# Kernel optimization log

Measured on AMD Instinct MI355X. Metric: run time of the kernel, lower is better.

Reference implementation:

```python
import jax, jax.numpy as jnp
import numpy as np
from jax import lax

EPS = 1e-5
F_CH = 32  # TIM future channels = int(256/8)
B_CH = 32  # TIM past channels (note: source bug -> these are zeroed, not shifted)


def inorm(x):
    # InstanceNorm3d (no affine): normalize each (b, c) over (T, H, W), biased var
    m = jnp.mean(x, axis=(2, 3, 4), keepdims=True)
    v = jnp.var(x, axis=(2, 3, 4), keepdims=True)
    return (x - m) * lax.rsqrt(v + EPS)


def conv1x1(x, w):
    # pointwise conv: x [B,C,T,H,W], w [O,C]
    return jnp.einsum('bcthw,oc->bothw', x, w)


def dwconv(x, w, pad):
    # depthwise 3D conv; w [C,1,kd,kh,kw], pad = [(pd,pd),(ph,ph),(pw,pw)]
    return lax.conv_general_dilated(
        x, w, window_strides=(1, 1, 1), padding=pad,
        feature_group_count=x.shape[1],
        dimension_numbers=('NCDHW', 'OIDHW', 'NCDHW'))


def tim(x):
    # Non-circular temporal interlacing. Faithful to source (past slice is a no-op):
    # channels [0:f]  <- x shifted from future (t+1), zero-padded at last frame
    # channels [f:f+b] <- zeros
    # channels [f+b:] <- identity
    f, b = F_CH, B_CH
    fut = jnp.concatenate([x[:, :f, 1:], jnp.zeros_like(x[:, :f, :1])], axis=2)
    mid = jnp.zeros_like(x[:, f:f + b])
    return jnp.concatenate([fut, mid, x[:, f + b:]], axis=1)


def setup_inputs() -> dict:
    key = jax.random.key(0)
    ks = jax.random.split(key, 7)
    cin, hid, cout = 64, 256, 64
    x = jax.random.normal(ks[0], (4, cin, 16, 64, 64), dtype=jnp.float32)
    w1 = jax.random.normal(ks[1], (hid, cin), dtype=jnp.float32) * 0.05
    w_dw_s = jax.random.normal(ks[2], (hid, 1, 1, 3, 3), dtype=jnp.float32) * 0.1
    w_dw_t = jax.random.normal(ks[3], (hid, 1, 3, 1, 1), dtype=jnp.float32) * 0.1
    w_se1 = jax.random.normal(ks[4], (hid // 4, hid), dtype=jnp.float32) * 0.05
    w_se2 = jax.random.normal(ks[5], (hid, hid // 4), dtype=jnp.float32) * 0.05
    w_proj = jax.random.normal(ks[6], (cout, hid), dtype=jnp.float32) * 0.05
    return {'x': x, 'w1': w1, 'w_dw_s': w_dw_s, 'w_dw_t': w_dw_t,
            'w_se1': w_se1, 'w_se2': w_se2, 'w_proj': w_proj}


def reference(x, w1, w_dw_s, w_dw_t, w_se1, w_se2, w_proj):
    shortcut = x
    # stage1: expand 1x1 conv + IN + ReLU
    h = jax.nn.relu(inorm(conv1x1(x, w1)))
    # temporal interlace (zero-FLOP channel shift)
    h = tim(h)
    # stage2: depthwise spatial (1,3,3) + IN + ReLU
    h = jax.nn.relu(inorm(dwconv(h, w_dw_s, [(0, 0), (1, 1), (1, 1)])))
    # stage3: depthwise temporal (3,1,1) + IN + ReLU
    h = jax.nn.relu(inorm(dwconv(h, w_dw_t, [(1, 1), (0, 0), (0, 0)])))
    # squeeze-excite
    y = jnp.mean(h, axis=(2, 3, 4), keepdims=True)           # [B,C,1,1,1]
    y = jax.nn.relu(jnp.einsum('bcthw,oc->bothw', y, w_se1))
    y = jax.nn.sigmoid(jnp.einsum('bcthw,oc->bothw', y, w_se2))
    h = h * y
    # proj 1x1 + IN, residual, maxpool (1,2,2)
    out = inorm(conv1x1(h, w_proj)) + shortcut
    out = lax.reduce_window(out, -jnp.inf, lax.max,
                            (1, 1, 1, 2, 2), (1, 1, 1, 2, 2), 'VALID')
    return out
```

## Files before the change

kernel.cpp:

```cpp
#include <hip/hip_runtime.h>
#include <hip/hip_bf16.h>

#define B_   4
#define CIN  64
#define HID  256
#define COUT 64
#define T_   16
#define H_   64
#define W_   64
#define HW_  (H_*W_)
#define THW  (T_*HW_)
#define EPS  1e-5f

typedef unsigned short ushort_t;
typedef unsigned int   uint_t;
typedef short bf16x8 __attribute__((ext_vector_type(8)));
typedef float f32x4  __attribute__((ext_vector_type(4)));

#define SM3   4096
#define SIS3  5120
#define SSES  6144
#define SAL   7168
#define SBE   8192
__device__ float g_stats[10240];
__device__ float g_eps [4*1024*256];
__device__ float g_epss[4*1024*256];
__device__ float g_pps [4*64*512];
__device__ float g_ppss[4*64*512];
__device__ ushort_t g_wpack[32768];

__device__ __forceinline__ float bf2f(ushort_t u) {
    return __uint_as_float(((uint_t)u) << 16);
}
__device__ __forceinline__ ushort_t f2bf(float f) {
    uint_t u = __float_as_uint(f);
    uint_t r = u + 0x7fffu + ((u >> 16) & 1u);
    return (ushort_t)(r >> 16);
}
__device__ __forceinline__ void unpacknorm2(uint2 k, float a, float bb, float* v) {
    uint_t uu[2] = {k.x, k.y};
    #pragma unroll
    for (int j = 0; j < 2; ++j) {
        v[2*j]   = fmaxf(fmaf(__uint_as_float(uu[j] << 16),         a, bb), 0.f);
        v[2*j+1] = fmaxf(fmaf(__uint_as_float(uu[j] & 0xffff0000u), a, bb), 0.f);
    }
}

__global__ __launch_bounds__(256) void k_prep(const float* __restrict__ w1,
                                              const float* __restrict__ wproj) {
    int idx = blockIdx.x*256 + threadIdx.x;
    {
        int j = idx & 7, lane = (idx>>3) & 63, ot = (idx>>9) & 3;
        int ks = (idx>>11) & 1, wv = idx >> 12;
        int ln = lane & 15, q = lane >> 4;
        int o = wv*64 + ot*16 + ln, k = ks*32 + q*8 + j;
        g_wpack[idx] = f2bf(w1[o*CIN + k]);
    }
    {
        int j = idx & 7, lane = (idx>>3) & 63, ot = (idx>>9) & 3, kg = idx >> 11;
        int ln = lane & 15, q = lane >> 4;
        int o = ot*16 + ln, k = kg*32 + q*8 + j;
        g_wpack[16384 + idx] = f2bf(wproj[o*HID + k]);
    }
}

__global__ __launch_bounds__(256) void k_expand(const float* __restrict__ x,
                                                ushort_t* __restrict__ h1, int b0) {
    union SMem {
        ushort_t Bs[64*72];
        float    red[2][256][16];
    };
    __shared__ SMem sm;
    const int tid = threadIdx.x;
    const int bb  = blockIdx.y, gb = b0 + bb;
    const int pos0 = blockIdx.x * 64;
    const int lane = tid & 63, wv = tid >> 6;
    const int q = lane >> 4, ln = lane & 15;

    bf16x8 af[2][4];
    #pragma unroll
    for (int ks = 0; ks < 2; ++ks)
        #pragma unroll
        for (int ot = 0; ot < 4; ++ot)
            af[ks][ot] = *(const bf16x8*)&g_wpack[(((wv*2+ks)*4+ot)<<9) + lane*8];

    #pragma unroll
    for (int i = 0; i < 4; ++i) {
        int lin = i*1024 + tid*4;
        int k = lin >> 6, n0 = lin & 63;
        float4 v = *(const float4*)&x[(size_t)(gb*CIN + k) * THW + pos0 + n0];
        ushort_t* d = &sm.Bs[k*72 + ((n0 + 16*((k>>3)&3)) & 63)];
        d[0] = f2bf(v.x); d[1] = f2bf(v.y); d[2] = f2bf(v.z); d[3] = f2bf(v.w);
    }
    __syncthreads();

    f32x4 acc[4][4];
    #pragma unroll
    for (int i = 0; i < 4; ++i)
        #pragma unroll
        for (int j = 0; j < 4; ++j)
            acc[i][j] = (f32x4){0.f,0.f,0.f,0.f};

    #pragma unroll
    for (int ks = 0; ks < 2; ++ks) {
        bf16x8 bfr[4];
        #pragma unroll
        for (int nt = 0; nt < 4; ++nt) {
            union { short s[8]; bf16x8 v; } bu;
            #pragma unroll
            for (int j = 0; j < 8; ++j) {
                int k = ks*32 + q*8 + j;
                int nn = (nt*16 + ln + 16*((k>>3)&3)) & 63;
                bu.s[j] = (short)sm.Bs[k*72 + nn];
            }
            bfr[nt] = bu.v;
        }
        #pragma unroll
        for (int ot = 0; ot < 4; ++ot)
            #pragma unroll
            for (int nt = 0; nt < 4; ++nt)
                acc[ot][nt] = __builtin_amdgcn_mfma_f32_16x16x32_bf16(
                    af[ks][ot], bfr[nt], acc[ot][nt], 0, 0, 0);
    }

    float sp_[16], ssp_[16];
    #pragma unroll
    for (int i = 0; i < 16; ++i) { sp_[i] = 0.f; ssp_[i] = 0.f; }

    #pragma unroll
    for (int ot = 0; ot < 4; ++ot)
        #pragma unroll
        for (int nt = 0; nt < 4; ++nt)
            #pragma unroll
            for (int r = 0; r < 4; ++r) {
                float vv = acc[ot][nt][r];
                int o = wv*64 + ot*16 + q*4 + r;
                int n = nt*16 + ln;
                h1[((size_t)bb*HID + o)*THW + pos0 + n] = f2bf(vv);
                sp_[ot*4+r] += vv;
                ssp_[ot*4+r] = fmaf(vv, vv, ssp_[ot*4+r]);
            }

    __syncthreads();
    #pragma unroll
    for (int i = 0; i < 16; ++i) {
        int o = wv*64 + (i>>2)*16 + q*4 + (i&3);
        sm.red[0][o][ln] = sp_[i];
        sm.red[1][o][ln] = ssp_[i];
    }
    __syncthreads();
    {
        float s = 0.f, ss = 0.f;
        #pragma unroll
        for (int l = 0; l < 16; ++l) {
            s  += sm.red[0][tid][l];
            ss += sm.red[1][tid][l];
        }
        size_t base = ((size_t)bb*1024 + blockIdx.x)*256 + tid;
        g_eps [base] = s;
        g_epss[base] = ss;
    }
}

__global__ __launch_bounds__(1024) void k_mid(const ushort_t* __restrict__ h1,
                                              const float* __restrict__ wdws,
                                              const float* __restrict__ wdwt,
                                              ushort_t* __restrict__ h3) {
    const int tid = threadIdx.x;
    const int bc  = blockIdx.x;
    const int o   = bc & (HID-1);
    const int bb  = bc >> 8;
    const int wid = tid >> 6, lane = tid & 63;

    if (o >= 32 && o < 64) {
        if (tid == 0) {
            g_stats[SM3  + bc] = 0.f;
            g_stats[SIS3 + bc] = 1.f / sqrtf(EPS);
            g_stats[SSES + bc] = 0.f;
        }
        return;
    }

    __shared__ float pl[2][66*67];
    __shared__ float ls[16], lss[16];
    __shared__ float sa, sb;

    {
        const float* ps  = &g_eps [((size_t)bb*1024)*256 + o];
        const float* pss = &g_epss[((size_t)bb*1024)*256 + o];
        float s  = ps [(size_t)tid*256];
        float ss = pss[(size_t)tid*256];
        #pragma unroll
        for (int m = 32; m > 0; m >>= 1) {
            s  += __shfl_xor(s,  m);
            ss += __shfl_xor(ss, m);
        }
        if (lane == 0) { ls[wid] = s; lss[wid] = ss; }
        if (tid < 66) {
            #pragma unroll
            for (int b = 0; b < 2; ++b) {
                pl[b][tid]         = 0.f;
                pl[b][65*67 + tid] = 0.f;
                pl[b][tid*67]      = 0.f;
                pl[b][tid*67 + 65] = 0.f;
            }
        }
        __syncthreads();
        if (tid == 0) {
            float st = 0.f, sst = 0.f;
            #pragma unroll
            for (int i = 0; i < 16; ++i) { st += ls[i]; sst += lss[i]; }
            float m = st * (1.f/THW);
            float v = sst * (1.f/THW) - m*m;
            float is = 1.f / sqrtf(v + EPS);
            sa = is; sb = -m * is;
        }
        __syncthreads();
    }
    const float a1 = sa, b1 = sb;

    const int fut = (o < 32) ? 1 : 0;
    const int y   = tid >> 4;
    const int x0  = (tid & 15) * 4;
    const ushort_t* chp = h1 + (size_t)bc * THW;
    const int lastp = fut ? (T_-2) : (T_-1);

    float wf[9];
    #pragma unroll
    for (int k = 0; k < 9; ++k) wf[k] = wdws[o*9 + k];

    uint2 sreg[2];
    sreg[0] = *(const uint2*)(chp + (size_t)fut*HW_ + tid*4);
    {
        float vv[4];
        unpacknorm2(sreg[0], a1, b1, vv);
        float* dst = &pl[0][(y+1)*67 + x0 + 1];
        #pragma unroll
        for (int i = 0; i < 4; ++i) dst[i] = vv[i];
    }
    sreg[1] = *(const uint2*)(chp + (size_t)(1+fut)*HW_ + tid*4);
    __syncthreads();

    uint2 keep[16];
    float s2 = 0.f, ss2 = 0.f;

    #pragma unroll
    for (int t = 0; t < T_; ++t) {
        if (t + 2 <= lastp)
            sreg[t & 1] = *(const uint2*)(chp + (size_t)(t+2+fut)*HW_ + tid*4);
        if (t + 1 <= lastp) {
            float vv[4];
            unpacknorm2(sreg[(t+1) & 1], a1, b1, vv);
            float* dst = &pl[(t+1) & 1][(y+1)*67 + x0 + 1];
            #pragma unroll
            for (int i = 0; i < 4; ++i) dst[i] = vv[i];
        }
        if (fut && t == T_-1) {
            keep[t] = (uint2){0u, 0u};
        } else {
            const float* plane = pl[t & 1];
            float v[3][6];
            #pragma unroll
            for (int dy = 0; dy < 3; ++dy) {
                const float* rp = &plane[(y + dy)*67 + x0];
                #pragma unroll
                for (int j = 0; j < 6; ++j) v[dy][j] = rp[j];
            }
            uint_t outp[2];
            #pragma unroll
            for (int i2 = 0; i2 < 2; ++i2) {
                float o0 = 0.f, o1 = 0.f;
                #pragma unroll
                for (int dy = 0; dy < 3; ++dy)
                    #pragma unroll
                    for (int dx = 0; dx < 3; ++dx) {
                        float w = wf[dy*3+dx];
                        o0 = fmaf(w, v[dy][2*i2 + dx],     o0);
                        o1 = fmaf(w, v[dy][2*i2 + 1 + dx], o1);
                    }
                ushort_t u0 = f2bf(o0), u1 = f2bf(o1);
                float r0 = bf2f(u0), r1 = bf2f(u1);
                s2 += r0 + r1; ss2 = fmaf(r0, r0, fmaf(r1, r1, ss2));
                outp[i2] = (uint_t)u0 | ((uint_t)u1 << 16);
            }
            keep[t].x = outp[0]; keep[t].y = outp[1];
        }
        __syncthreads();
    }

    {
        float s = s2, ss = ss2;
        #pragma unroll
        for (int m = 32; m > 0; m >>= 1) {
            s  += __shfl_xor(s,  m);
            ss += __shfl_xor(ss, m);
        }
        if (lane == 0) { ls[wid] = s; lss[wid] = ss; }
        __syncthreads();
        if (tid == 0) {
            float st = 0.f, sst = 0.f;
            #pragma unroll
            for (int i = 0; i < 16; ++i) { st += ls[i]; sst += lss[i]; }
            float m = st * (1.f/THW);
            float v = sst * (1.f/THW) - m*m;
            float is = 1.f / sqrtf(v + EPS);
            sa = is; sb = -m * is;
        }
        __syncthreads();
    }
    const float a2 = sa, b2 = sb;

    const float w0 = wdwt[o*3+0], w1 = wdwt[o*3+1], w2 = wdwt[o*3+2];
    ushort_t* op = h3 + (size_t)bc * THW + tid*4;

    float p[4], c[4], n[4];
    #pragma unroll
    for (int i = 0; i < 4; ++i) p[i] = 0.f;
    unpacknorm2(keep[0], a2, b2, c);
    unpacknorm2(keep[1], a2, b2, n);

    float s3 = 0.f, ss3 = 0.f;
    #pragma unroll
    for (int t = 0; t < T_; ++t) {
        uint_t outp[2];
        #pragma unroll
        for (int i2 = 0; i2 < 2; ++i2) {
            float o0 = fmaf(w0, p[2*i2],   fmaf(w1, c[2*i2],   w2 * n[2*i2]));
            float o1 = fmaf(w0, p[2*i2+1], fmaf(w1, c[2*i2+1], w2 * n[2*i2+1]));
            ushort_t u0 = f2bf(o0), u1 = f2bf(o1);
            float r0 = bf2f(u0), r1 = bf2f(u1);
            s3 += r0 + r1; ss3 = fmaf(r0, r0, fmaf(r1, r1, ss3));
            outp[i2] = (uint_t)u0 | ((uint_t)u1 << 16);
        }
        uint2 r; r.x = outp[0]; r.y = outp[1];
        *(uint2*)(op + (size_t)t*HW_) = r;

        #pragma unroll
        for (int i = 0; i < 4; ++i) { p[i] = c[i]; c[i] = n[i]; }
        if (t + 2 < T_) unpacknorm2(keep[t+2], a2, b2, n);
        else {
            #pragma unroll
            for (int i = 0; i < 4; ++i) n[i] = 0.f;
        }
        keep[t] = r;
    }

    {
        float s = s3, ss = ss3;
        #pragma unroll
        for (int m = 32; m > 0; m >>= 1) {
            s  += __shfl_xor(s,  m);
            ss += __shfl_xor(ss, m);
        }
        if (lane == 0) { ls[wid] = s; lss[wid] = ss; }
        __syncthreads();
        if (tid == 0) {
            float st = 0.f, sst = 0.f;
            #pragma unroll
            for (int i = 0; i < 16; ++i) { st += ls[i]; sst += lss[i]; }
            float m = st * (1.f/THW);
            float v = sst * (1.f/THW) - m*m;
            float is = 1.f / sqrtf(v + EPS);
            g_stats[SM3  + bc] = m;
            g_stats[SIS3 + bc] = is;
            sa = is; sb = -m * is;
        }
        __syncthreads();
    }

    const float a3 = sa, b3 = sb;
    float sse = 0.f;
    #pragma unroll
    for (int t = 0; t < T_; ++t) {
        uint_t uu[2] = {keep[t].x, keep[t].y};
        #pragma unroll
        for (int j = 0; j < 2; ++j) {
            sse += fmaxf(fmaf(__uint_as_float(uu[j] << 16),         a3, b3), 0.f);
            sse += fmaxf(fmaf(__uint_as_float(uu[j] & 0xffff0000u), a3, b3), 0.f);
        }
    }
    #pragma unroll
    for (int m = 32; m > 0; m >>= 1) sse += __shfl_xor(sse, m);
    if (lane == 0) ls[wid] = sse;
    __syncthreads();
    if (tid == 0) {
        float st = 0.f;
        #pragma unroll
        for (int i = 0; i < 16; ++i) st += ls[i];
        g_stats[SSES + bc] = st * (1.f/THW);
    }
}

__global__ __launch_bounds__(256) void k_semlp(const float* __restrict__ wse1,
                                               const float* __restrict__ wse2) {
    __shared__ float mv[HID];
    __shared__ float y1[64];
    const int bb = blockIdx.x, tid = threadIdx.x;
    mv[tid] = g_stats[SSES + bb*HID + tid];
    __syncthreads();
    if (tid < 64) {
        float acc = 0.f;
        #pragma unroll 8
        for (int c = 0; c < HID; ++c) acc = fmaf(wse1[tid*HID + c], mv[c], acc);
        y1[tid] = fmaxf(acc, 0.f);
    }
    __syncthreads();
    float z = 0.f;
    #pragma unroll
    for (int c = 0; c < 64; ++c) z = fmaf(wse2[tid*64 + c], y1[c], z);
    float se = 1.f / (1.f + expf(-z));
    const int bc = bb*HID + tid;
    float al = g_stats[SIS3 + bc] * se;
    if (tid >= 32 && tid < 64) al = 0.f;
    g_stats[SAL + bc] = al;
    g_stats[SBE + bc] = -g_stats[SM3 + bc] * al;
}

__global__ __launch_bounds__(256) void k_proj(const ushort_t* __restrict__ h3,
                                              float* __restrict__ proj) {
    __shared__ ushort_t Bs[64*136];
    __shared__ float rs[64][4], rss[64][4];
    const int tid = threadIdx.x;
    const int bb  = blockIdx.y;
    const int pos0 = blockIdx.x * 128;
    const int lane = tid & 63, wv = tid >> 6;
    const int q = lane >> 4, ln = lane & 15;

    f32x4 acc[4][2];
    #pragma unroll
    for (int i = 0; i < 4; ++i) {
        acc[i][0] = (f32x4){0.f,0.f,0.f,0.f};
        acc[i][1] = (f32x4){0.f,0.f,0.f,0.f};
    }

    for (int kc = 0; kc < 4; ++kc) {
        #pragma unroll
        for (int i = 0; i < 8; ++i) {
            int lin = i*1024 + tid*4;
            int kl = lin >> 7, n0 = lin & 127;
            int ch = bb*HID + kc*64 + kl;
            float al = g_stats[SAL + ch], be = g_stats[SBE + ch];
            ushort_t* d = &Bs[kl*136 + ((n0 + 16*((kl>>3)&7)) & 127)];
            if (al == 0.f) {
                d[0] = 0; d[1] = 0; d[2] = 0; d[3] = 0;
            } else {
                uint2 u = *(const uint2*)&h3[(size_t)ch * THW + pos0 + n0];
                float f0 = __uint_as_float(u.x << 16);
                float f1 = __uint_as_float(u.x & 0xffff0000u);
                float f2 = __uint_as_float(u.y << 16);
                float f3 = __uint_as_float(u.y & 0xffff0000u);
                d[0] = f2bf(fmaxf(fmaf(f0, al, be), 0.f));
                d[1] = f2bf(fmaxf(fmaf(f1, al, be), 0.f));
                d[2] = f2bf(fmaxf(fmaf(f2, al, be), 0.f));
                d[3] = f2bf(fmaxf(fmaf(f3, al, be), 0.f));
            }
        }
        __syncthreads();

        #pragma unroll
        for (int ks = 0; ks < 2; ++ks) {
            int kg = kc*2 + ks;
            bf16x8 af[4];
            #pragma unroll
            for (int ot = 0; ot < 4; ++ot)
                af[ot] = *(const bf16x8*)&g_wpack[16384 + ((kg*4+ot)<<9) + lane*8];
            bf16x8 bfr[2];
            #pragma unroll
            for (int nt = 0; nt < 2; ++nt) {
                union { short s[8]; bf16x8 v; } bu;
                #pragma unroll
                for (int j = 0; j < 8; ++j) {
                    int kl = ks*32 + q*8 + j;
                    int nn = (wv*32 + nt*16 + ln + 16*((kl>>3)&7)) & 127;
                    bu.s[j] = (short)Bs[kl*136 + nn];
                }
                bfr[nt] = bu.v;
            }
            #pragma unroll
            for (int ot = 0; ot < 4; ++ot)
                #pragma unroll
                for (int nt = 0; nt < 2; ++nt)
                    acc[ot][nt] = __builtin_amdgcn_mfma_f32_16x16x32_bf16(
                        af[ot], bfr[nt], acc[ot][nt], 0, 0, 0);
        }
        __syncthreads();
    }

    #pragma unroll
    for (int ot = 0; ot < 4; ++ot)
        #pragma unroll
        for (int nt = 0; nt < 2; ++nt)
            #pragma unroll
            for (int r = 0; r < 4; ++r) {
                int o = ot*16 + q*4 + r;
                int n = wv*32 + nt*16 + ln;
                proj[((size_t)bb*COUT + o)*THW + pos0 + n] = acc[ot][nt][r];
            }

    #pragma unroll
    for (int ot = 0; ot < 4; ++ot)
        #pragma unroll
        for (int r = 0; r < 4; ++r) {
            float s  = acc[ot][0][r] + acc[ot][1][r];
            float ss = fmaf(acc[ot][0][r], acc[ot][0][r],
                            acc[ot][1][r] * acc[ot][1][r]);
            #pragma unroll
            for (int m = 1; m < 16; m <<= 1) {
                s  += __shfl_xor(s,  m);
                ss += __shfl_xor(ss, m);
            }
            if (ln == 0) {
                int o = ot*16 + q*4 + r;
                rs[o][wv]  = s;
                rss[o][wv] = ss;
            }
        }
    __syncthreads();
    if (tid < 64) {
        float s  = rs[tid][0]  + rs[tid][1]  + rs[tid][2]  + rs[tid][3];
        float ss = rss[tid][0] + rss[tid][1] + rss[tid][2] + rss[tid][3];
        size_t base = ((size_t)bb*64 + tid)*512 + blockIdx.x;
        g_pps [base] = s;
        g_ppss[base] = ss;
    }
}

__global__ __launch_bounds__(1024) void k_final(const float* __restrict__ proj,
                                                const float* __restrict__ x,
                                                float* __restrict__ out, int b0) {
    const int bo  = blockIdx.x;
    const int tid = threadIdx.x;
    const float* p = proj + (size_t)bo * THW;

    float s = 0.f, ss = 0.f;
    if (tid < 512) {
        s  = g_pps [(size_t)bo*512 + tid];
        ss = g_ppss[(size_t)bo*512 + tid];
    }
    #pragma unroll
    for (int off = 32; off > 0; off >>= 1) {
        s  += __shfl_down(s,  off, 64);
        ss += __shfl_down(ss, off, 64);
    }
    __shared__ float ls[16], lss[16];
    __shared__ float sa, sb;
    int wid = tid >> 6, lane = tid & 63;
    if (lane == 0) { ls[wid] = s; lss[wid] = ss; }
    __syncthreads();
    if (tid == 0) {
        float st = 0.f, sst = 0.f;
        #pragma unroll
        for (int i = 0; i < 16; ++i) { st += ls[i]; sst += lss[i]; }
        float m = st * (1.f/THW);
        float v = sst * (1.f/THW) - m*m;
        float is = 1.f / sqrtf(v + EPS);
        sa = is; sb = -m * is;
    }
    __syncthreads();
    const float a = sa, bb = sb;

    const size_t gbase = (size_t)(b0*COUT + bo) * THW;
    float* op = out + (size_t)(b0*COUT + bo) * (T_*1024);
    #pragma unroll
    for (int i = 0; i < 16; ++i) {
        int idx = i*1024 + tid;
        int xx = idx & 31, yy = (idx >> 5) & 31, t = idx >> 10;
        float m = -3.4e38f;
        #pragma unroll
        for (int r = 0; r < 2; ++r) {
            size_t off = (size_t)t*HW_ + (size_t)(2*yy + r)*W_ + 2*xx;
            float2 p2 = *(const float2*)(p + off);
            float2 x2 = *(const float2*)(x + gbase + off);
            float v0 = fmaf(p2.x, a, bb) + x2.x;
            float v1 = fmaf(p2.y, a, bb) + x2.y;
            m = fmaxf(m, fmaxf(v0, v1));
        }
        op[idx] = m;
    }
}

extern "C" void kernel_launch(void* const* d_in, const int* in_sizes, int n_in,
                              void* d_out, int out_size, void* d_ws, size_t ws_size,
                              hipStream_t stream) {
    const float* x     = (const float*)d_in[0];
    const float* w1    = (const float*)d_in[1];
    const float* wdws  = (const float*)d_in[2];
    const float* wdwt  = (const float*)d_in[3];
    const float* wse1  = (const float*)d_in[4];
    const float* wse2  = (const float*)d_in[5];
    const float* wproj = (const float*)d_in[6];
    float* out = (float*)d_out;

    const size_t perb = 2ull * HID * THW * sizeof(ushort_t);
    int nb = (ws_size >= 4*perb) ? 4 : (ws_size >= 2*perb) ? 2 : 1;

    k_prep<<<64, 256, 0, stream>>>(w1, wproj);

    for (int b0 = 0; b0 < B_; b0 += nb) {
        char* ws = (char*)d_ws;
        ushort_t* h1   = (ushort_t*)ws;
        ushort_t* h3   = h1;
        float*    proj = (float*)(ws + (size_t)nb * HID*THW*2);

        k_expand<<<dim3(THW/64, nb), 256, 0, stream>>>(x, h1, b0);
        k_mid   <<<nb*HID, 1024, 0, stream>>>(h1, wdws, wdwt, h3);
        k_semlp <<<nb, 256, 0, stream>>>(wse1, wse2);
        k_proj  <<<dim3(THW/128, nb), 256, 0, stream>>>(h3, proj);
        k_final <<<nb*COUT, 1024, 0, stream>>>(proj, x, out, b0);
    }
}
```

Before: 376.3 us.

## Move stage-1 stat reduction to separate kernel and recompute proj stats in final

Adds a k_red kernel that reduces the per-block expand partial sums into per-channel normalization scale and shift before k_mid, so the 1024-thread k_mid blocks no longer each do a strided gather and two block barriers. k_proj no longer computes and writes partial sums of its output. k_final instead recomputes the mean and variance by re-reading the whole projection channel from memory. This trades an extra launch and an extra pass over the proj data for a lighter GEMM epilogue and a lighter k_mid prologue.

```diff
diff --git a/kernel.cpp b/kernel.cpp
--- a/kernel.cpp
+++ b/kernel.cpp
@@ -17,6 +17,8 @@
 typedef short bf16x8 __attribute__((ext_vector_type(8)));
 typedef float f32x4  __attribute__((ext_vector_type(4)));
 
+#define SA1   0
+#define SB1   1024
 #define SM3   4096
 #define SIS3  5120
 #define SSES  6144
@@ -25,8 +27,6 @@
 __device__ float g_stats[10240];
 __device__ float g_eps [4*1024*256];
 __device__ float g_epss[4*1024*256];
-__device__ float g_pps [4*64*512];
-__device__ float g_ppss[4*64*512];
 __device__ ushort_t g_wpack[32768];
 
 __device__ __forceinline__ float bf2f(ushort_t u) {
@@ -162,6 +162,37 @@
     }
 }
 
+__global__ __launch_bounds__(256) void k_red() {
+    const int tid = threadIdx.x;
+    const int cg  = blockIdx.x;
+    const int bb  = blockIdx.y;
+    const int ch  = cg*16 + (tid & 15);
+    const int pb0 = tid >> 4;
+    const float* ps  = &g_eps [((size_t)bb*1024)*256];
+    const float* pss = &g_epss[((size_t)bb*1024)*256];
+    float s = 0.f, ss = 0.f;
+    #pragma unroll 8
+    for (int it = 0; it < 64; ++it) {
+        int pb = it*16 + pb0;
+        s  += ps [(size_t)pb*256 + ch];
+        ss += pss[(size_t)pb*256 + ch];
+    }
+    __shared__ float rs[256], rss[256];
+    rs[tid] = s; rss[tid] = ss;
+    __syncthreads();
+    if (tid < 16) {
+        float st = 0.f, sst = 0.f;
+        #pragma unroll
+        for (int k = 0; k < 16; ++k) { st += rs[tid + 16*k]; sst += rss[tid + 16*k]; }
+        float m = st * (1.f/THW);
+        float v = sst * (1.f/THW) - m*m;
+        float is = 1.f / sqrtf(v + EPS);
+        int bc = bb*HID + cg*16 + tid;
+        g_stats[SA1 + bc] = is;
+        g_stats[SB1 + bc] = -m * is;
+    }
+}
+
 __global__ __launch_bounds__(1024) void k_mid(const ushort_t* __restrict__ h1,
                                               const float* __restrict__ wdws,
                                               const float* __restrict__ wdwt,
@@ -185,39 +216,18 @@
     __shared__ float ls[16], lss[16];
     __shared__ float sa, sb;
 
-    {
-        const float* ps  = &g_eps [((size_t)bb*1024)*256 + o];
-        const float* pss = &g_epss[((size_t)bb*1024)*256 + o];
-        float s  = ps [(size_t)tid*256];
-        float ss = pss[(size_t)tid*256];
-        #pragma unroll
-        for (int m = 32; m > 0; m >>= 1) {
-            s  += __shfl_xor(s,  m);
-            ss += __shfl_xor(ss, m);
-        }
-        if (lane == 0) { ls[wid] = s; lss[wid] = ss; }
-        if (tid < 66) {
-            #pragma unroll
-            for (int b = 0; b < 2; ++b) {
-                pl[b][tid]         = 0.f;
-                pl[b][65*67 + tid] = 0.f;
-                pl[b][tid*67]      = 0.f;
-                pl[b][tid*67 + 65] = 0.f;
-            }
-        }
-        __syncthreads();
-        if (tid == 0) {
-            float st = 0.f, sst = 0.f;
-            #pragma unroll
-            for (int i = 0; i < 16; ++i) { st += ls[i]; sst += lss[i]; }
-            float m = st * (1.f/THW);
-            float v = sst * (1.f/THW) - m*m;
-            float is = 1.f / sqrtf(v + EPS);
-            sa = is; sb = -m * is;
-        }
-        __syncthreads();
-    }
-    const float a1 = sa, b1 = sb;
+    const float a1 = g_stats[SA1 + bc];
+    const float b1 = g_stats[SB1 + bc];
+
+    if (tid < 66) {
+        #pragma unroll
+        for (int b = 0; b < 2; ++b) {
+            pl[b][tid]         = 0.f;
+            pl[b][65*67 + tid] = 0.f;
+            pl[b][tid*67]      = 0.f;
+            pl[b][tid*67 + 65] = 0.f;
+        }
+    }
 
     const int fut = (o < 32) ? 1 : 0;
     const int y   = tid >> 4;
@@ -419,7 +429,6 @@
 __global__ __launch_bounds__(256) void k_proj(const ushort_t* __restrict__ h3,
                                               float* __restrict__ proj) {
     __shared__ ushort_t Bs[64*136];
-    __shared__ float rs[64][4], rss[64][4];
     const int tid = threadIdx.x;
     const int bb  = blockIdx.y;
     const int pos0 = blockIdx.x * 128;
@@ -496,33 +505,6 @@
                 int n = wv*32 + nt*16 + ln;
                 proj[((size_t)bb*COUT + o)*THW + pos0 + n] = acc[ot][nt][r];
             }
-
-    #pragma unroll
-    for (int ot = 0; ot < 4; ++ot)
-        #pragma unroll
-        for (int r = 0; r < 4; ++r) {
-            float s  = acc[ot][0][r] + acc[ot][1][r];
-            float ss = fmaf(acc[ot][0][r], acc[ot][0][r],
-                            acc[ot][1][r] * acc[ot][1][r]);
-            #pragma unroll
-            for (int m = 1; m < 16; m <<= 1) {
-                s  += __shfl_xor(s,  m);
-                ss += __shfl_xor(ss, m);
-            }
-            if (ln == 0) {
-                int o = ot*16 + q*4 + r;
-                rs[o][wv]  = s;
-                rss[o][wv] = ss;
-            }
-        }
-    __syncthreads();
-    if (tid < 64) {
-        float s  = rs[tid][0]  + rs[tid][1]  + rs[tid][2]  + rs[tid][3];
-        float ss = rss[tid][0] + rss[tid][1] + rss[tid][2] + rss[tid][3];
-        size_t base = ((size_t)bb*64 + tid)*512 + blockIdx.x;
-        g_pps [base] = s;
-        g_ppss[base] = ss;
-    }
 }
 
 __global__ __launch_bounds__(1024) void k_final(const float* __restrict__ proj,
@@ -533,9 +515,13 @@
     const float* p = proj + (size_t)bo * THW;
 
     float s = 0.f, ss = 0.f;
-    if (tid < 512) {
-        s  = g_pps [(size_t)bo*512 + tid];
-        ss = g_ppss[(size_t)bo*512 + tid];
+    #pragma unroll
+    for (int i = 0; i < THW/(1024*4); ++i) {
+        float4 u = *(const float4*)(p + i*4096 + tid*4);
+        s += u.x; ss = fmaf(u.x, u.x, ss);
+        s += u.y; ss = fmaf(u.y, u.y, ss);
+        s += u.z; ss = fmaf(u.z, u.z, ss);
+        s += u.w; ss = fmaf(u.w, u.w, ss);
     }
     #pragma unroll
     for (int off = 32; off > 0; off >>= 1) {
@@ -603,6 +589,7 @@
         float*    proj = (float*)(ws + (size_t)nb * HID*THW*2);
 
         k_expand<<<dim3(THW/64, nb), 256, 0, stream>>>(x, h1, b0);
+        k_red   <<<dim3(16, nb), 256, 0, stream>>>();
         k_mid   <<<nb*HID, 1024, 0, stream>>>(h1, wdws, wdwt, h3);
         k_semlp <<<nb, 256, 0, stream>>>(wse1, wse2);
         k_proj  <<<dim3(THW/128, nb), 256, 0, stream>>>(h3, proj);
```

Measured after the change: 354.9 us. -5.7%, faster.
